# Optimization experiments

Hardware: AMD Instinct MI355X
Metric: run time of the kernel (lower is better)

Reference implementation:

```python
import jax, jax.numpy as jnp
import numpy as np

B, L_SEQ = 2, 2048
D, H, DF, NL, V = 1024, 16, 4096, 3, 32000
E = D // H
EPS = 1e-5


def _ln(x, g, b):
    m = jnp.mean(x, axis=-1, keepdims=True)
    v = jnp.mean((x - m) ** 2, axis=-1, keepdims=True)
    return (x - m) * jax.lax.rsqrt(v + EPS) * g + b


def setup_inputs() -> dict:
    key = jax.random.key(0)
    ks = jax.random.split(key, 16)
    s = 0.02
    tokens = jax.random.randint(ks[0], (B, L_SEQ), 0, V)
    pad_mask = jnp.zeros((B, L_SEQ, 1), dtype=bool)
    inp = dict(
        tokens=tokens,
        pad_mask=pad_mask,
        tok_emb=jax.random.normal(ks[1], (V, D)) * s,
        pos_emb=jax.random.normal(ks[2], (L_SEQ, D)) * s,
        Wq=jax.random.normal(ks[3], (NL, D, D)) * s,
        bq=jnp.zeros((NL, D)),
        Wk=jax.random.normal(ks[4], (NL, D, D)) * s,
        bk=jnp.zeros((NL, D)),
        Wv=jax.random.normal(ks[5], (NL, D, D)) * s,
        bv=jnp.zeros((NL, D)),
        Wo=jax.random.normal(ks[6], (NL, D, D)) * s,
        bo=jnp.zeros((NL, D)),
        W1=jax.random.normal(ks[7], (NL, D, DF)) * s,
        b1=jnp.zeros((NL, DF)),
        W2=jax.random.normal(ks[8], (NL, DF, D)) * s,
        b2=jnp.zeros((NL, D)),
        ln1_g=jnp.ones((NL, D)), ln1_b=jnp.zeros((NL, D)),
        ln3_g=jnp.ones((NL, D)), ln3_b=jnp.zeros((NL, D)),
        lnf_g=jnp.ones((D,)), lnf_b=jnp.zeros((D,)),
        Wout=jax.random.normal(ks[9], (D, V)) * s,
        bout=jnp.zeros((V,)),
    )
    return inp


def reference(tokens, pad_mask, tok_emb, pos_emb, Wq, bq, Wk, bk, Wv, bv,
              Wo, bo, W1, b1, W2, b2, ln1_g, ln1_b, ln3_g, ln3_b,
              lnf_g, lnf_b, Wout, bout):
    Bb, Ls = tokens.shape
    x = tok_emb[tokens] + pos_emb[:Ls]  # [B,L,D]
    causal = jnp.triu(jnp.ones((Ls, Ls), dtype=bool), 1)
    # pad mask applied on keys, causal on (query,key); mask True = blocked
    mask = jnp.logical_or(pad_mask[:, :, 0][:, None, :], causal[None])  # [B,L,L]
    mask = mask[:, None]  # [B,1,L,L], broadcast over heads
    scale = 1.0 / np.sqrt(E)
    for i in range(NL):
        h = _ln(x, ln1_g[i], ln1_b[i])
        q = (h @ Wq[i] + bq[i]).reshape(Bb, Ls, H, E)
        k = (h @ Wk[i] + bk[i]).reshape(Bb, Ls, H, E)
        v = (h @ Wv[i] + bv[i]).reshape(Bb, Ls, H, E)
        scores = jnp.einsum('blhe,bshe->bhls', q, k)
        scores = jnp.where(mask, -jnp.inf, scores)
        A = jax.nn.softmax(scale * scores, axis=-1)
        A = jnp.where(mask, 0.0, A)
        o = jnp.einsum('bhls,bshd->blhd', A, v).reshape(Bb, Ls, D)
        x = x + (o @ Wo[i] + bo[i])
        h = _ln(x, ln3_g[i], ln3_b[i])
        h = jax.nn.gelu(h @ W1[i] + b1[i], approximate=False)
        x = x + (h @ W2[i] + b2[i])
    x = _ln(x, lnf_g, lnf_b)
    return x @ Wout + bout  # [B,L,V]
```

## Files before the change

kernel.cpp:

```cpp
#include <hip/hip_runtime.h>
#include <math.h>

#define D_    1024
#define H_    16
#define E_    64
#define DF_   4096
#define NL_   3
#define V_    32000
#define B_    2
#define LSEQ_ 2048
#define M_    (B_*LSEQ_)
#define QKVW  (3*D_)

#define OQKV  0
#define OWO   ((size_t)3072*1024)
#define OW1   ((size_t)4096*1024)
#define OW2   ((size_t)8192*1024)

typedef __attribute__((ext_vector_type(8))) short bf16x8;
typedef __attribute__((ext_vector_type(4))) float f32x4;
typedef __attribute__((ext_vector_type(4))) unsigned short us4_t;

__device__ __forceinline__ float bfr2f(unsigned short u){ return __uint_as_float(((unsigned)u)<<16); }
__device__ __forceinline__ unsigned short f2bfr(float f){
  unsigned u = __float_as_uint(f);
  u += 0x7fffu + ((u>>16)&1u);
  return (unsigned short)(u>>16);
}
__device__ __forceinline__ void gl_lds16(const unsigned short* g, unsigned short* l){
  __builtin_amdgcn_global_load_lds((const __attribute__((address_space(1))) void*)g,
                                   (__attribute__((address_space(3))) void*)l, 16, 0, 0);
}
__device__ __forceinline__ float fast_erf(float x){
  float xa = fabsf(x);
  float tt = __frcp_rn(1.f + 0.3275911f*xa);
  float poly = tt*(0.254829592f + tt*(-0.284496736f + tt*(1.421413741f +
               tt*(-1.453152027f + tt*1.061405429f))));
  float er = 1.f - poly*__expf(-xa*xa);
  return copysignf(er, x);
}

__device__ __forceinline__ void row_ln_write(float4 v, const float* __restrict__ g,
                                             const float* __restrict__ b,
                                             unsigned short* __restrict__ hrow,
                                             float* red, int tid){
  const int wave = tid>>6, lane = tid&63;
  float s  = v.x+v.y+v.z+v.w;
  float s2 = v.x*v.x+v.y*v.y+v.z*v.z+v.w*v.w;
  #pragma unroll
  for (int off=1; off<64; off<<=1){ s += __shfl_xor(s,off); s2 += __shfl_xor(s2,off); }
  if (!lane){ red[wave]=s; red[4+wave]=s2; }
  __syncthreads();
  s  = red[0]+red[1]+red[2]+red[3];
  s2 = red[4]+red[5]+red[6]+red[7];
  const float mean = s*(1.f/D_);
  const float var  = s2*(1.f/D_) - mean*mean;
  const float rstd = rsqrtf(var + 1e-5f);
  float4 gg = ((const float4*)g)[tid];
  float4 bb = ((const float4*)b)[tid];
  us4_t ov;
  ov[0] = f2bfr((v.x-mean)*rstd*gg.x + bb.x);
  ov[1] = f2bfr((v.y-mean)*rstd*gg.y + bb.y);
  ov[2] = f2bfr((v.z-mean)*rstd*gg.z + bb.z);
  ov[3] = f2bfr((v.w-mean)*rstd*gg.w + bb.w);
  *(us4_t*)&hrow[tid*4] = ov;
}

__global__ __launch_bounds__(256) void embed_ln_kernel(const int* __restrict__ tokens,
                                                       const float* __restrict__ tok_emb,
                                                       const float* __restrict__ pos_emb,
                                                       const float* __restrict__ g,
                                                       const float* __restrict__ b,
                                                       const float* __restrict__ bq,
                                                       const float* __restrict__ bk,
                                                       const float* __restrict__ bv,
                                                       float* __restrict__ bqkv3,
                                                       float* __restrict__ x,
                                                       unsigned short* __restrict__ h){
  __shared__ float red[8];
  const int r = blockIdx.x, tid = threadIdx.x;
  if (r < NL_*QKVW/256){
    int i = r*256 + tid;
    int layer = i / QKVW, j = i % QKVW;
    bqkv3[i] = (j < D_) ? bq[layer*D_+j] : (j < 2*D_) ? bk[layer*D_+j-D_] : bv[layer*D_+j-2*D_];
  }
  const int l = r & (LSEQ_-1);
  const int t = tokens[r];
  float4 te = ((const float4*)(tok_emb + (size_t)t*D_))[tid];
  float4 pe = ((const float4*)(pos_emb + (size_t)l*D_))[tid];
  float4 o = {te.x+pe.x, te.y+pe.y, te.z+pe.z, te.w+pe.w};
  ((float4*)(x + (size_t)r*D_))[tid] = o;
  row_ln_write(o, g, b, h + (size_t)r*D_, red, tid);
}

__global__ __launch_bounds__(256) void ln_kernel(const float* __restrict__ x,
                                                 const float* __restrict__ g,
                                                 const float* __restrict__ b,
                                                 unsigned short* __restrict__ h){
  __shared__ float red[8];
  const int r = blockIdx.x, tid = threadIdx.x;
  float4 v = ((const float4*)(x + (size_t)r*D_))[tid];
  row_ln_write(v, g, b, h + (size_t)r*D_, red, tid);
}

__global__ __launch_bounds__(256) void reduce2_ln_kernel(float* __restrict__ x,
                                                         const float* __restrict__ pt,
                                                         const float* __restrict__ bias,
                                                         const float* __restrict__ g,
                                                         const float* __restrict__ b,
                                                         unsigned short* __restrict__ h){
  __shared__ float red[8];
  const int r = blockIdx.x, tid = threadIdx.x;
  const size_t i = ((size_t)r*D_ + tid*4);
  float4 xv = *(const float4*)(x + i);
  float4 p0 = *(const float4*)(pt + i);
  float4 p1 = *(const float4*)(pt + (size_t)M_*D_ + i);
  float4 bb = *(const float4*)(bias + tid*4);
  xv.x += p0.x + p1.x + bb.x;
  xv.y += p0.y + p1.y + bb.y;
  xv.z += p0.z + p1.z + bb.z;
  xv.w += p0.w + p1.w + bb.w;
  *(float4*)(x + i) = xv;
  row_ln_write(xv, g, b, h + (size_t)r*D_, red, tid);
}

__global__ __launch_bounds__(256) void transpose_layer_kernel(const float* __restrict__ Wq,
                                                              const float* __restrict__ Wk,
                                                              const float* __restrict__ Wv,
                                                              const float* __restrict__ Wo,
                                                              const float* __restrict__ W1,
                                                              const float* __restrict__ W2,
                                                              unsigned short* __restrict__ wt){
  __shared__ unsigned short T[64*65];
  const int tid = threadIdx.x;
  const int rr = tid>>4, c4 = (tid&15)*4;
  const int nr = tid>>2, kc = (tid&3)*16;
  auto params = [&](int t, const float*& W, unsigned short*& dst, int& N, int& K, int& n0, int& k0){
    if (t < 768){
      int z = t>>8, tt = t&255;
      W = (z==0)?Wq:(z==1)?Wk:Wv; N=1024; K=1024;
      n0=(tt&15)*64; k0=(tt>>4)*64;
      dst = wt + OQKV + (size_t)z*1024*1024;
    } else if (t < 1024){
      int tt = t-768; W=Wo; N=1024; K=1024;
      n0=(tt&15)*64; k0=(tt>>4)*64; dst = wt + OWO;
    } else if (t < 2048){
      int tt = t-1024; W=W1; N=4096; K=1024;
      n0=(tt&63)*64; k0=(tt>>6)*64; dst = wt + OW1;
    } else {
      int tt = t-2048; W=W2; N=1024; K=4096;
      n0=(tt&15)*64; k0=(tt>>4)*64; dst = wt + OW2;
    }
  };
  auto loadRegs = [&](int t, float4* r){
    const float* W; unsigned short* dst; int N, K, n0, k0;
    params(t, W, dst, N, K, n0, k0);
    #pragma unroll
    for (int pp=0; pp<4; pp++)
      r[pp] = *(const float4*)(W + (size_t)(k0+pp*16+rr)*N + n0 + c4);
  };
  float4 r[4];
  loadRegs(blockIdx.x*4, r);
  #pragma unroll
  for (int i=0; i<4; i++){
    float4 rn[4];
    if (i<3) loadRegs(blockIdx.x*4 + i + 1, rn);
    #pragma unroll
    for (int pp=0; pp<4; pp++){
      int row = pp*16 + rr;
      T[(c4+0)*65 + row] = f2bfr(r[pp].x);
      T[(c4+1)*65 + row] = f2bfr(r[pp].y);
      T[(c4+2)*65 + row] = f2bfr(r[pp].z);
      T[(c4+3)*65 + row] = f2bfr(r[pp].w);
    }
    __syncthreads();
    {
      const float* W; unsigned short* dst; int N, K, n0, k0;
      params(blockIdx.x*4 + i, W, dst, N, K, n0, k0);
      bf16x8 o0, o1;
      #pragma unroll
      for (int j=0;j<8;j++){ o0[j] = (short)T[nr*65 + kc + j];
                             o1[j] = (short)T[nr*65 + kc + 8 + j]; }
      *(bf16x8*)&dst[(size_t)(n0+nr)*K + k0 + kc]     = o0;
      *(bf16x8*)&dst[(size_t)(n0+nr)*K + k0 + kc + 8] = o1;
    }
    if (i<3){
      __syncthreads();
      #pragma unroll
      for (int pp=0; pp<4; pp++) r[pp] = rn[pp];
    }
  }
}

__global__ __launch_bounds__(256) void transpose_wout_kernel(const float* __restrict__ W,
                                                             unsigned short* __restrict__ WT){
  __shared__ unsigned short T[64*65];
  const int tid = threadIdx.x;
  const int rr = tid>>4, c4 = (tid&15)*4;
  const int nr = tid>>2, kc = (tid&3)*16;
  auto loadRegs = [&](int t, float4* r){
    int n0 = (t%500)*64, k0 = (t/500)*64;
    #pragma unroll
    for (int pp=0; pp<4; pp++)
      r[pp] = *(const float4*)(W + (size_t)(k0+pp*16+rr)*V_ + n0 + c4);
  };
  float4 r[4];
  loadRegs(blockIdx.x*4, r);
  #pragma unroll
  for (int i=0; i<4; i++){
    float4 rn[4];
    if (i<3) loadRegs(blockIdx.x*4 + i + 1, rn);
    #pragma unroll
    for (int pp=0; pp<4; pp++){
      int row = pp*16 + rr;
      T[(c4+0)*65 + row] = f2bfr(r[pp].x);
      T[(c4+1)*65 + row] = f2bfr(r[pp].y);
      T[(c4+2)*65 + row] = f2bfr(r[pp].z);
      T[(c4+3)*65 + row] = f2bfr(r[pp].w);
    }
    __syncthreads();
    {
      int t = blockIdx.x*4 + i;
      int n0 = (t%500)*64, k0 = (t/500)*64;
      bf16x8 o0, o1;
      #pragma unroll
      for (int j=0;j<8;j++){ o0[j] = (short)T[nr*65 + kc + j];
                             o1[j] = (short)T[nr*65 + kc + 8 + j]; }
      *(bf16x8*)&WT[(size_t)(n0+nr)*D_ + k0 + kc]     = o0;
      *(bf16x8*)&WT[(size_t)(n0+nr)*D_ + k0 + kc + 8] = o1;
    }
    if (i<3){
      __syncthreads();
      #pragma unroll
      for (int pp=0; pp<4; pp++) r[pp] = rn[pp];
    }
  }
}

template<int EPI>
__global__ __launch_bounds__(256) void gemm_bt(const unsigned short* __restrict__ A,
                                               const unsigned short* __restrict__ Bt,
                                               const float* __restrict__ bias,
                                               unsigned short* __restrict__ Cb,
                                               float* __restrict__ Cf,
                                               int K, int Klen, int ldc){
  __shared__ unsigned short As[128*64];
  __shared__ unsigned short Bs[128*64];
  const int tid = threadIdx.x;
  const int wave = tid>>6, lane = tid&63;
  const int m0 = blockIdx.x*128, n0 = blockIdx.y*128;
  const int kbase = blockIdx.z * Klen;
  const int wr = wave>>1, wc = wave&1;
  const unsigned short* Ab = A + (size_t)m0*K + kbase;
  const unsigned short* Bb = Bt + (size_t)n0*K + kbase;
  f32x4 acc[4][4] = {};
  int srow[4], sk[4];
  #pragma unroll
  for (int i=0;i<4;i++){
    int ci = i*256 + tid;
    srow[i] = ci>>3;
    sk[i]   = ((ci&7) ^ (srow[i]&7))*8;
  }
  for (int kt=0; kt<Klen; kt+=64){
    __syncthreads();
    #pragma unroll
    for (int i=0;i<4;i++){
      gl_lds16(Ab + (size_t)srow[i]*K + kt + sk[i], As + i*2048 + wave*512);
      gl_lds16(Bb + (size_t)srow[i]*K + kt + sk[i], Bs + i*2048 + wave*512);
    }
    __syncthreads();
    #pragma unroll
    for (int ks=0; ks<2; ks++){
      bf16x8 af[4], bfv[4];
      #pragma unroll
      for (int mi=0;mi<4;mi++){
        int row = wr*64 + mi*16 + (lane&15);
        int ch  = (ks*4 + (lane>>4)) ^ (row&7);
        af[mi] = *(const bf16x8*)&As[row*64 + ch*8];
      }
      #pragma unroll
      for (int ni=0;ni<4;ni++){
        int row = wc*64 + ni*16 + (lane&15);
        int ch  = (ks*4 + (lane>>4)) ^ (row&7);
        bfv[ni] = *(const bf16x8*)&Bs[row*64 + ch*8];
      }
      #pragma unroll
      for (int mi=0;mi<4;mi++)
        #pragma unroll
        for (int ni=0;ni<4;ni++)
          acc[mi][ni] = __builtin_amdgcn_mfma_f32_16x16x32_bf16(af[mi], bfv[ni], acc[mi][ni], 0,0,0);
    }
  }
  const int rq = (lane>>4)*4, cq = lane&15;
  float* Cfz = (EPI==5) ? (Cf + (size_t)blockIdx.z*M_*D_) : Cf;
  #pragma unroll
  for (int mi=0;mi<4;mi++){
    #pragma unroll
    for (int j=0;j<4;j++){
      int r = m0 + wr*64 + mi*16 + rq + j;
      #pragma unroll
      for (int ni=0;ni<4;ni++){
        int c = n0 + wc*64 + ni*16 + cq;
        if (EPI==2)      Cf[(size_t)r*D_ + c] += acc[mi][ni][j] + bias[c];
        else if (EPI==5) Cfz[(size_t)r*ldc + c] = acc[mi][ni][j];
        else             Cf[(size_t)r*ldc + c] = acc[mi][ni][j] + bias[c];
      }
    }
  }
}

#define GBAR()  do{ __builtin_amdgcn_s_barrier(); __builtin_amdgcn_sched_barrier(0); }while(0)
#define GPHASE(P, STAGE_STMT, TAIL_STMT) do{                                        \
    bf16x8 afr[2][2];                                                               \
    _Pragma("unroll")                                                               \
    for (int mi=0;mi<2;mi++){                                                       \
      _Pragma("unroll")                                                             \
      for (int ks=0;ks<2;ks++){                                                     \
        int row = wr*128 + (P)*32 + mi*16 + (lane&15);                              \
        int ch  = (ks*4 + (lane>>4)) ^ (row&7);                                     \
        afr[mi][ks] = *(const bf16x8*)&Alds[row*64 + ch*8];                         \
      } }                                                                           \
    STAGE_STMT;                                                                     \
    GBAR();                                                                         \
    asm volatile("s_waitcnt lgkmcnt(0)" ::: "memory");                              \
    __builtin_amdgcn_sched_barrier(0);                                              \
    __builtin_amdgcn_s_setprio(1);                                                  \
    _Pragma("unroll")                                                               \
    for (int ks=0;ks<2;ks++){                                                       \
      _Pragma("unroll")                                                             \
      for (int mi=0;mi<2;mi++){                                                     \
        _Pragma("unroll")                                                           \
        for (int ni=0;ni<4;ni++)                                                    \
          acc[(P)*2+mi][ni] = __builtin_amdgcn_mfma_f32_16x16x32_bf16(              \
              afr[mi][ks], bfr[ni][ks], acc[(P)*2+mi][ni], 0,0,0);                  \
      } }                                                                           \
    __builtin_amdgcn_s_setprio(0);                                                  \
    __builtin_amdgcn_sched_barrier(0);                                              \
    TAIL_STMT;                                                                      \
  }while(0)

template<int EPI>
__global__ __launch_bounds__(512, 2) void gemm256(const unsigned short* __restrict__ A,
                                                  const unsigned short* __restrict__ Bt,
                                                  const float* __restrict__ bias,
                                                  unsigned short* __restrict__ Cb,
                                                  float* __restrict__ Cf,
                                                  int K, int ldc){
  __shared__ unsigned short lds[2][2][256*64];
  const int tid = threadIdx.x, wave = tid>>6, lane = tid&63;
  const int m0 = blockIdx.x*256, n0 = blockIdx.y*256;
  const int wr = wave>>2, wc = wave&3;
  const unsigned short* Ab = A  + (size_t)m0*K;
  const unsigned short* Bb = Bt + (size_t)n0*K;
  int srow[2], scol[2];
  #pragma unroll
  for (int i=0;i<2;i++){
    int ci = i*512 + tid;
    srow[i] = ci>>3;
    scol[i] = ((ci&7) ^ (srow[i]&7))*8;
  }
  auto stageA = [&](int tbuf, int hh, int kt){
    #pragma unroll
    for (int i=0;i<2;i++)
      gl_lds16(Ab + (size_t)(hh*128+srow[i])*K + kt + scol[i],
               &lds[tbuf][0][hh*8192 + (i*512+tid)*8]);
  };
  auto stageB = [&](int tbuf, int hh, int kt){
    #pragma unroll
    for (int i=0;i<2;i++)
      gl_lds16(Bb + (size_t)(hh*128+srow[i])*K + kt + scol[i],
               &lds[tbuf][1][hh*8192 + (i*512+tid)*8]);
  };
  f32x4 acc[8][4] = {};
  const int NT = K>>6;
  stageB(0,0,0); stageB(0,1,0);
  stageA(0,0,0); stageA(0,1,0);
  stageB(1,0,64); stageB(1,1,64);
  asm volatile("s_waitcnt vmcnt(4)" ::: "memory");
  __builtin_amdgcn_sched_barrier(0);
  GBAR();
  for (int t=0; t<NT; ++t){
    const int buf = t&1, bufn = buf^1;
    const unsigned short* Alds = &lds[buf][0][0];
    const unsigned short* Blds = &lds[buf][1][0];
    const int ktA = (t+1)<<6, ktB = (t+2)<<6;
    const bool s1 = (t+1)<NT, s2 = (t+2)<NT;
    bf16x8 bfr[4][2];
    #pragma unroll
    for (int ni=0;ni<4;ni++)
      #pragma unroll
      for (int ks=0;ks<2;ks++){
        int row = wc*64 + ni*16 + (lane&15);
        int ch  = (ks*4 + (lane>>4)) ^ (row&7);
        bfr[ni][ks] = *(const bf16x8*)&Blds[row*64 + ch*8];
      }
    GPHASE(0, if (s1) stageA(bufn,0,ktA), ((void)0));
    GPHASE(1, if (s1) stageA(bufn,1,ktA), ((void)0));
    GPHASE(2, if (s2) stageB(buf,0,ktB), ((void)0));
    GPHASE(3, if (s2) stageB(buf,1,ktB),
           { if (s2){ asm volatile("s_waitcnt vmcnt(4)" ::: "memory"); }
             else   { asm volatile("s_waitcnt vmcnt(0)" ::: "memory"); }
             __builtin_amdgcn_sched_barrier(0);
             GBAR(); });
  }
  const int rq = (lane>>4)*4, cq = lane&15;
  const float qsc = (EPI==0 && blockIdx.y < 4) ? 0.18033688f : 1.0f;
  #pragma unroll
  for (int mi=0;mi<8;mi++){
    #pragma unroll
    for (int j=0;j<4;j++){
      int r = m0 + wr*128 + mi*16 + rq + j;
      #pragma unroll
      for (int ni=0;ni<4;ni++){
        int c = n0 + wc*64 + ni*16 + cq;
        float v = acc[mi][ni][j] + bias[c];
        if (EPI==0)      Cb[(size_t)r*ldc + c] = f2bfr(v*qsc);
        else if (EPI==1) Cb[(size_t)r*ldc + c] = f2bfr(0.5f*v*(1.f+fast_erf(v*0.70710678f)));
        else             Cf[(size_t)r*ldc + c] = v;
      }
    }
  }
}

__global__ __launch_bounds__(512) void attn_kernel(const unsigned short* __restrict__ qkv,
                                                   unsigned short* __restrict__ o){
  int bid = blockIdx.x, qt, bh;
  if (bid < 256){ qt = bid & 15;        bh = bid >> 4; }
  else          { qt = 15 - (bid & 15); bh = 16 + ((bid - 256) >> 4); }
  const int b = bh>>4, h = bh&15;
  const int tid = threadIdx.x, wave = tid>>6, lane = tid&63;
  const int ql0 = qt*128;
  __shared__ unsigned short Qs[128*64];
  __shared__ unsigned short Ks[2][64*64];
  __shared__ unsigned short Vt[2][80*72];
  __shared__ unsigned short Ps[128*72];
  const size_t base = (size_t)b*LSEQ_*QKVW + (size_t)h*E_;
  const unsigned short* qb = qkv + base;
  const unsigned short* kb = qkv + base + D_;
  const unsigned short* vb = qkv + base + 2*D_;
  #pragma unroll
  for (int ii=0; ii<2; ii++){
    int i = wave + ii*8;
    int chunk = i*64 + lane, r = chunk>>3, cc = chunk&7;
    gl_lds16(qb + (size_t)(ql0 + r)*QKVW + ((cc^(r&7))*8), Qs + i*512);
  }
  for (int i = tid; i < 2*16*72; i += 512){
    int bufi = (i >= 16*72);
    int rem  = i - bufi*16*72;
    Vt[bufi][(64 + rem/72)*72 + (rem%72)] = 0x3F80;
  }
  const int kck = wave*64 + lane, kr = kck>>3, kc = kck&7;
  gl_lds16(kb + (size_t)kr*QKVW + ((kc^(kr&7))*8), &Ks[0][wave*512]);
  {
    bf16x8 vv = *(const bf16x8*)(vb + (size_t)lane*QKVW + wave*8);
    #pragma unroll
    for (int j=0;j<8;j++) Vt[0][(wave*8+j)*72 + lane] = (unsigned short)vv[j];
  }
  __syncthreads();
  bf16x8 qf[2];
  {
    int qrow = wave*16 + (lane&15);
    #pragma unroll
    for (int ks=0; ks<2; ks++){
      int qc = ks*4 + (lane>>4);
      qf[ks] = *(const bf16x8*)&Qs[qrow*64 + ((qc^(qrow&7))*8)];
    }
  }
  float m4[4] = {-3e38f,-3e38f,-3e38f,-3e38f};
  f32x4 oacc[5] = {};
  const int nkv = qt*2 + 2;
  for (int t=0; t<nkv; t++){
    const int s0 = t*64, cur = t&1, nxt = cur^1;
    const bool more = (t+1) < nkv;
    bf16x8 vvn;
    if (more){
      const int s0n = s0 + 64;
      gl_lds16(kb + (size_t)(s0n + kr)*QKVW + ((kc^(kr&7))*8), &Ks[nxt][wave*512]);
      vvn = *(const bf16x8*)(vb + (size_t)(s0n + lane)*QKVW + wave*8);
    }
    __builtin_amdgcn_sched_barrier(0);
    f32x4 sacc[4] = {};
    __builtin_amdgcn_s_setprio(1);
    #pragma unroll
    for (int ks=0; ks<2; ks++){
      #pragma unroll
      for (int fc=0; fc<4; fc++){
        int krow = fc*16 + (lane&15);
        int qc = ks*4 + (lane>>4);
        bf16x8 bv = *(const bf16x8*)&Ks[cur][krow*64 + ((qc^(krow&7))*8)];
        sacc[fc] = __builtin_amdgcn_mfma_f32_16x16x32_bf16(qf[ks], bv, sacc[fc], 0,0,0);
      }
    }
    __builtin_amdgcn_s_setprio(0);
    float rm[4];
    if (s0 + 63 > ql0 + wave*16){
      #pragma unroll
      for (int j=0;j<4;j++){
        int rowa = ql0 + wave*16 + (lane>>4)*4 + j;
        float mx = -3e38f;
        #pragma unroll
        for (int fc=0;fc<4;fc++){
          int cola = s0 + fc*16 + (lane&15);
          if (cola > rowa) sacc[fc][j] = -3e38f;
          mx = fmaxf(mx, sacc[fc][j]);
        }
        rm[j] = mx;
      }
    } else {
      #pragma unroll
      for (int j=0;j<4;j++){
        float mx = fmaxf(fmaxf(sacc[0][j], sacc[1][j]), fmaxf(sacc[2][j], sacc[3][j]));
        rm[j] = mx;
      }
    }
    #pragma unroll
    for (int off=1; off<16; off<<=1)
      #pragma unroll
      for (int j=0;j<4;j++) rm[j] = fmaxf(rm[j], __shfl_xor(rm[j], off));
    bool need = (rm[0]>m4[0]+11.5f)||(rm[1]>m4[1]+11.5f)||(rm[2]>m4[2]+11.5f)||(rm[3]>m4[3]+11.5f);
    const bool rescale = (__ballot(need) != 0ull);
    if (rescale){
      float al[4];
      #pragma unroll
      for (int j=0;j<4;j++){
        float mn = fmaxf(m4[j], rm[j]);
        al[j] = exp2f(m4[j] - mn);
        m4[j] = mn;
      }
      #pragma unroll
      for (int fc=0;fc<5;fc++)
        #pragma unroll
        for (int j=0;j<4;j++) oacc[fc][j] *= al[j];
    }
    #pragma unroll
    for (int fc=0;fc<4;fc++)
      #pragma unroll
      for (int j=0;j<4;j++){
        float pv = exp2f(sacc[fc][j] - m4[j]);
        Ps[(wave*16 + (lane>>4)*4 + j)*72 + fc*16 + (lane&15)] =
            (unsigned short)(__float_as_uint(pv)>>16);
      }
    __builtin_amdgcn_s_setprio(1);
    #pragma unroll
    for (int ks=0; ks<2; ks++){
      bf16x8 ap = *(const bf16x8*)&Ps[(wave*16 + (lane&15))*72 + ks*32 + (lane>>4)*8];
      #pragma unroll
      for (int fc=0;fc<5;fc++){
        bf16x8 bv = *(const bf16x8*)&Vt[cur][(fc*16 + (lane&15))*72 + ks*32 + (lane>>4)*8];
        oacc[fc] = __builtin_amdgcn_mfma_f32_16x16x32_bf16(ap, bv, oacc[fc], 0,0,0);
      }
    }
    __builtin_amdgcn_s_setprio(0);
    if (more){
      #pragma unroll
      for (int j=0;j<8;j++) Vt[nxt][(wave*8+j)*72 + lane] = (unsigned short)vvn[j];
    }
    __syncthreads();
  }
  #pragma unroll
  for (int fc=0;fc<4;fc++)
    #pragma unroll
    for (int j=0;j<4;j++){
      int r = ql0 + wave*16 + (lane>>4)*4 + j;
      int c = h*E_ + fc*16 + (lane&15);
      o[((size_t)b*LSEQ_ + r)*D_ + c] = f2bfr(oacc[fc][j] / oacc[4][j]);
    }
}

extern "C" void kernel_launch(void* const* d_in, const int* in_sizes, int n_in,
                              void* d_out, int out_size, void* d_ws, size_t ws_size,
                              hipStream_t stream){
  (void)in_sizes; (void)n_in; (void)out_size;
  const int*   tokens = (const int*)d_in[0];
  const float* tok_emb= (const float*)d_in[2];
  const float* pos_emb= (const float*)d_in[3];
  const float* Wq = (const float*)d_in[4];
  const float* bq = (const float*)d_in[5];
  const float* Wk = (const float*)d_in[6];
  const float* bk = (const float*)d_in[7];
  const float* Wv = (const float*)d_in[8];
  const float* bv = (const float*)d_in[9];
  const float* Wo = (const float*)d_in[10];
  const float* bo = (const float*)d_in[11];
  const float* W1 = (const float*)d_in[12];
  const float* b1 = (const float*)d_in[13];
  const float* W2 = (const float*)d_in[14];
  const float* b2 = (const float*)d_in[15];
  const float* ln1g = (const float*)d_in[16];
  const float* ln1b = (const float*)d_in[17];
  const float* ln3g = (const float*)d_in[18];
  const float* ln3b = (const float*)d_in[19];
  const float* lnfg = (const float*)d_in[20];
  const float* lnfb = (const float*)d_in[21];
  const float* Wout = (const float*)d_in[22];
  const float* bout = (const float*)d_in[23];

  char* p = (char*)d_ws;
  float* x             = (float*)p;           p += (size_t)M_*D_*sizeof(float);
  unsigned short* h    = (unsigned short*)p;  p += (size_t)M_*D_*2;
  unsigned short* qkv  = (unsigned short*)p;  p += (size_t)M_*QKVW*2;
  unsigned short* ob   = (unsigned short*)p;  p += (size_t)M_*D_*2;
  unsigned short* ffh  = (unsigned short*)p;  p += (size_t)M_*DF_*2;
  unsigned short* wt   = (unsigned short*)p;  p += (size_t)V_*D_*2;
  float* bqkv3         = (float*)p;           p += (size_t)NL_*QKVW*sizeof(float);
  if ((size_t)(p - (char*)d_ws) > ws_size) return;
  float* pt = (float*)qkv;

  embed_ln_kernel<<<M_, 256, 0, stream>>>(tokens, tok_emb, pos_emb, ln1g, ln1b,
                                          bq, bk, bv, bqkv3, x, h);
  for (int i=0;i<NL_;i++){
    const size_t wOff  = (size_t)i*D_*D_;
    const size_t w1Off = (size_t)i*D_*DF_;
    transpose_layer_kernel<<<768, 256, 0, stream>>>(Wq + wOff, Wk + wOff, Wv + wOff,
                                                    Wo + wOff, W1 + w1Off, W2 + w1Off, wt);
    gemm256<0><<<dim3(M_/256, QKVW/256), 512, 0, stream>>>(h, wt + OQKV, bqkv3 + i*QKVW, qkv, nullptr, D_, QKVW);
    attn_kernel<<<512, 512, 0, stream>>>(qkv, ob);
    gemm_bt<2><<<dim3(M_/128, D_/128), 256, 0, stream>>>(ob, wt + OWO, bo + i*D_, nullptr, x, D_, D_, D_);
    ln_kernel<<<M_, 256, 0, stream>>>(x, ln3g + i*D_, ln3b + i*D_, h);
    gemm256<1><<<dim3(M_/256, DF_/256), 512, 0, stream>>>(h, wt + OW1, b1 + i*DF_, ffh, nullptr, D_, DF_);
    gemm_bt<5><<<dim3(M_/128, D_/128, 2), 256, 0, stream>>>(ffh, wt + OW2, nullptr, nullptr, pt, DF_, DF_/2, D_);
    reduce2_ln_kernel<<<M_, 256, 0, stream>>>(x, pt, b2 + i*D_,
                                              (i < NL_-1) ? ln1g + (i+1)*D_ : lnfg,
                                              (i < NL_-1) ? ln1b + (i+1)*D_ : lnfb, h);
  }
  transpose_wout_kernel<<<2000, 256, 0, stream>>>(Wout, wt);
  gemm256<3><<<dim3(M_/256, V_/256), 512, 0, stream>>>(h, wt, bout, nullptr, (float*)d_out, D_, V_);
}
```

Before: 1.092 ms.

## Batch all layer weight transposes into one launch; split-K Wo GEMM with fused reduce+LN

Measured after the change: 1.094 ms. Within noise of the previous version (+0.2%).

```diff
diff --git a/kernel.cpp b/kernel.cpp
--- a/kernel.cpp
+++ b/kernel.cpp
@@ -16,6 +16,7 @@
 #define OWO   ((size_t)3072*1024)
 #define OW1   ((size_t)4096*1024)
 #define OW2   ((size_t)8192*1024)
+#define LSLAB ((size_t)12*1024*1024)
 
 typedef __attribute__((ext_vector_type(8))) short bf16x8;
 typedef __attribute__((ext_vector_type(4))) float f32x4;
@@ -91,16 +92,6 @@
   float4 o = {te.x+pe.x, te.y+pe.y, te.z+pe.z, te.w+pe.w};
   ((float4*)(x + (size_t)r*D_))[tid] = o;
   row_ln_write(o, g, b, h + (size_t)r*D_, red, tid);
-}
-
-__global__ __launch_bounds__(256) void ln_kernel(const float* __restrict__ x,
-                                                 const float* __restrict__ g,
-                                                 const float* __restrict__ b,
-                                                 unsigned short* __restrict__ h){
-  __shared__ float red[8];
-  const int r = blockIdx.x, tid = threadIdx.x;
-  float4 v = ((const float4*)(x + (size_t)r*D_))[tid];
-  row_ln_write(v, g, b, h + (size_t)r*D_, red, tid);
 }
 
 __global__ __launch_bounds__(256) void reduce2_ln_kernel(float* __restrict__ x,
@@ -124,31 +115,36 @@
   row_ln_write(xv, g, b, h + (size_t)r*D_, red, tid);
 }
 
-__global__ __launch_bounds__(256) void transpose_layer_kernel(const float* __restrict__ Wq,
-                                                              const float* __restrict__ Wk,
-                                                              const float* __restrict__ Wv,
-                                                              const float* __restrict__ Wo,
-                                                              const float* __restrict__ W1,
-                                                              const float* __restrict__ W2,
-                                                              unsigned short* __restrict__ wt){
+__global__ __launch_bounds__(256) void transpose_all_kernel(const float* __restrict__ Wq,
+                                                            const float* __restrict__ Wk,
+                                                            const float* __restrict__ Wv,
+                                                            const float* __restrict__ Wo,
+                                                            const float* __restrict__ W1,
+                                                            const float* __restrict__ W2,
+                                                            unsigned short* __restrict__ wt3){
   __shared__ unsigned short T[64*65];
   const int tid = threadIdx.x;
+  const int L = blockIdx.x / 768;
+  const int tbase = (blockIdx.x % 768) * 4;
+  unsigned short* wt = wt3 + (size_t)L*LSLAB;
+  const size_t wOff  = (size_t)L*D_*D_;
+  const size_t w1Off = (size_t)L*D_*DF_;
   const int rr = tid>>4, c4 = (tid&15)*4;
   const int nr = tid>>2, kc = (tid&3)*16;
   auto params = [&](int t, const float*& W, unsigned short*& dst, int& N, int& K, int& n0, int& k0){
     if (t < 768){
       int z = t>>8, tt = t&255;
-      W = (z==0)?Wq:(z==1)?Wk:Wv; N=1024; K=1024;
+      W = ((z==0)?Wq:(z==1)?Wk:Wv) + wOff; N=1024; K=1024;
       n0=(tt&15)*64; k0=(tt>>4)*64;
       dst = wt + OQKV + (size_t)z*1024*1024;
     } else if (t < 1024){
-      int tt = t-768; W=Wo; N=1024; K=1024;
+      int tt = t-768; W=Wo+wOff; N=1024; K=1024;
       n0=(tt&15)*64; k0=(tt>>4)*64; dst = wt + OWO;
     } else if (t < 2048){
-      int tt = t-1024; W=W1; N=4096; K=1024;
+      int tt = t-1024; W=W1+w1Off; N=4096; K=1024;
       n0=(tt&63)*64; k0=(tt>>6)*64; dst = wt + OW1;
     } else {
-      int tt = t-2048; W=W2; N=1024; K=4096;
+      int tt = t-2048; W=W2+w1Off; N=1024; K=4096;
       n0=(tt&15)*64; k0=(tt>>4)*64; dst = wt + OW2;
     }
   };
@@ -160,11 +156,11 @@
       r[pp] = *(const float4*)(W + (size_t)(k0+pp*16+rr)*N + n0 + c4);
   };
   float4 r[4];
-  loadRegs(blockIdx.x*4, r);
+  loadRegs(tbase, r);
   #pragma unroll
   for (int i=0; i<4; i++){
     float4 rn[4];
-    if (i<3) loadRegs(blockIdx.x*4 + i + 1, rn);
+    if (i<3) loadRegs(tbase + i + 1, rn);
     #pragma unroll
     for (int pp=0; pp<4; pp++){
       int row = pp*16 + rr;
@@ -176,7 +172,7 @@
     __syncthreads();
     {
       const float* W; unsigned short* dst; int N, K, n0, k0;
-      params(blockIdx.x*4 + i, W, dst, N, K, n0, k0);
+      params(tbase + i, W, dst, N, K, n0, k0);
       bf16x8 o0, o1;
       #pragma unroll
       for (int j=0;j<8;j++){ o0[j] = (short)T[nr*65 + kc + j];
@@ -292,7 +288,7 @@
     }
   }
   const int rq = (lane>>4)*4, cq = lane&15;
-  float* Cfz = (EPI==5) ? (Cf + (size_t)blockIdx.z*M_*D_) : Cf;
+  float* Cfz = Cf + (size_t)blockIdx.z*M_*D_;
   #pragma unroll
   for (int mi=0;mi<4;mi++){
     #pragma unroll
@@ -301,9 +297,8 @@
       #pragma unroll
       for (int ni=0;ni<4;ni++){
         int c = n0 + wc*64 + ni*16 + cq;
-        if (EPI==2)      Cf[(size_t)r*D_ + c] += acc[mi][ni][j] + bias[c];
-        else if (EPI==5) Cfz[(size_t)r*ldc + c] = acc[mi][ni][j];
-        else             Cf[(size_t)r*ldc + c] = acc[mi][ni][j] + bias[c];
+        if (EPI==5) Cfz[(size_t)r*ldc + c] = acc[mi][ni][j];
+        else        Cf[(size_t)r*ldc + c] = acc[mi][ni][j] + bias[c];
       }
     }
   }
@@ -601,28 +596,27 @@
   unsigned short* qkv  = (unsigned short*)p;  p += (size_t)M_*QKVW*2;
   unsigned short* ob   = (unsigned short*)p;  p += (size_t)M_*D_*2;
   unsigned short* ffh  = (unsigned short*)p;  p += (size_t)M_*DF_*2;
-  unsigned short* wt   = (unsigned short*)p;  p += (size_t)V_*D_*2;
+  unsigned short* wt3  = (unsigned short*)p;  p += (size_t)NL_*LSLAB*2;
   float* bqkv3         = (float*)p;           p += (size_t)NL_*QKVW*sizeof(float);
   if ((size_t)(p - (char*)d_ws) > ws_size) return;
-  float* pt = (float*)qkv;
+  float* ptW2 = (float*)qkv;
+  float* ptWo = (float*)ffh;
 
   embed_ln_kernel<<<M_, 256, 0, stream>>>(tokens, tok_emb, pos_emb, ln1g, ln1b,
                                           bq, bk, bv, bqkv3, x, h);
+  transpose_all_kernel<<<NL_*768, 256, 0, stream>>>(Wq, Wk, Wv, Wo, W1, W2, wt3);
   for (int i=0;i<NL_;i++){
-    const size_t wOff  = (size_t)i*D_*D_;
-    const size_t w1Off = (size_t)i*D_*DF_;
-    transpose_layer_kernel<<<768, 256, 0, stream>>>(Wq + wOff, Wk + wOff, Wv + wOff,
-                                                    Wo + wOff, W1 + w1Off, W2 + w1Off, wt);
+    unsigned short* wt = wt3 + (size_t)i*LSLAB;
     gemm256<0><<<dim3(M_/256, QKVW/256), 512, 0, stream>>>(h, wt + OQKV, bqkv3 + i*QKVW, qkv, nullptr, D_, QKVW);
     attn_kernel<<<512, 512, 0, stream>>>(qkv, ob);
-    gemm_bt<2><<<dim3(M_/128, D_/128), 256, 0, stream>>>(ob, wt + OWO, bo + i*D_, nullptr, x, D_, D_, D_);
-    ln_kernel<<<M_, 256, 0, stream>>>(x, ln3g + i*D_, ln3b + i*D_, h);
+    gemm_bt<5><<<dim3(M_/128, D_/128, 2), 256, 0, stream>>>(ob, wt + OWO, nullptr, nullptr, ptWo, D_, D_/2, D_);
+    reduce2_ln_kernel<<<M_, 256, 0, stream>>>(x, ptWo, bo + i*D_, ln3g + i*D_, ln3b + i*D_, h);
     gemm256<1><<<dim3(M_/256, DF_/256), 512, 0, stream>>>(h, wt + OW1, b1 + i*DF_, ffh, nullptr, D_, DF_);
-    gemm_bt<5><<<dim3(M_/128, D_/128, 2), 256, 0, stream>>>(ffh, wt + OW2, nullptr, nullptr, pt, DF_, DF_/2, D_);
-    reduce2_ln_kernel<<<M_, 256, 0, stream>>>(x, pt, b2 + i*D_,
+    gemm_bt<5><<<dim3(M_/128, D_/128, 2), 256, 0, stream>>>(ffh, wt + OW2, nullptr, nullptr, ptW2, DF_, DF_/2, D_);
+    reduce2_ln_kernel<<<M_, 256, 0, stream>>>(x, ptW2, b2 + i*D_,
                                               (i < NL_-1) ? ln1g + (i+1)*D_ : lnfg,
                                               (i < NL_-1) ? ln1b + (i+1)*D_ : lnfb, h);
   }
-  transpose_wout_kernel<<<2000, 256, 0, stream>>>(Wout, wt);
-  gemm256<3><<<dim3(M_/256, V_/256), 512, 0, stream>>>(h, wt, bout, nullptr, (float*)d_out, D_, V_);
-}
+  transpose_wout_kernel<<<2000, 256, 0, stream>>>(Wout, wt3);
+  gemm256<3><<<dim3(M_/256, V_/256), 512, 0, stream>>>(h, wt3, bout, nullptr, (float*)d_out, D_, V_);
+}
```
